# Performance work log

Measured on AMD Instinct MI355X. Metric: run time of the kernel, lower is better.

## Reference

```python
import jax, jax.numpy as jnp
import numpy as np

B, S, I, H = 8, 2048, 8, 256
HEADS, HD = 4, 64
DECAY = 0.95


def _lstm_layer(x, w_ih, w_hh, b_ih, b_hh):
    # x: [B, S, in]; torch gate order i, f, g, o
    Hs = w_hh.shape[1]
    x_proj = jnp.einsum('bsi,gi->bsg', x, w_ih) + b_ih + b_hh  # [B,S,4H]
    def step(carry, xt):
        h, c = carry
        gates = xt + h @ w_hh.T
        i, f, g, o = jnp.split(gates, 4, axis=-1)
        c = jax.nn.sigmoid(f) * c + jax.nn.sigmoid(i) * jnp.tanh(g)
        h = jax.nn.sigmoid(o) * jnp.tanh(c)
        return (h, c), h
    h0 = jnp.zeros((x.shape[0], Hs), x.dtype)
    (_, _), hs = jax.lax.scan(step, (h0, h0), jnp.swapaxes(x_proj, 0, 1))
    return jnp.swapaxes(hs, 0, 1)  # [B,S,H]


def setup_inputs() -> dict:
    key = jax.random.key(0)
    ks = jax.random.split(key, 25)
    sc = lambda n: 1.0 / np.sqrt(n)
    d = {}
    d['x'] = jax.random.normal(ks[0], (B, S, I), jnp.float32)
    # LSTM layer 0 (in=I) and layer 1 (in=H)
    d['w_ih0'] = jax.random.uniform(ks[1], (4 * H, I), jnp.float32, -sc(H), sc(H))
    d['w_hh0'] = jax.random.uniform(ks[2], (4 * H, H), jnp.float32, -sc(H), sc(H))
    d['b_ih0'] = jax.random.uniform(ks[3], (4 * H,), jnp.float32, -sc(H), sc(H))
    d['b_hh0'] = jax.random.uniform(ks[4], (4 * H,), jnp.float32, -sc(H), sc(H))
    d['w_ih1'] = jax.random.uniform(ks[5], (4 * H, H), jnp.float32, -sc(H), sc(H))
    d['w_hh1'] = jax.random.uniform(ks[6], (4 * H, H), jnp.float32, -sc(H), sc(H))
    d['b_ih1'] = jax.random.uniform(ks[7], (4 * H,), jnp.float32, -sc(H), sc(H))
    d['b_hh1'] = jax.random.uniform(ks[8], (4 * H,), jnp.float32, -sc(H), sc(H))
    # attention projections [H,H] (+bias)
    for i, n in enumerate(['q', 'k', 'v', 'o']):
        d['w' + n] = jax.random.normal(ks[9 + 2 * i], (H, H), jnp.float32) * sc(H)
        d['b' + n] = jnp.zeros((H,), jnp.float32)
    # dual heads [5,H]
    d['w_mean'] = jax.random.normal(ks[20], (5, H), jnp.float32) * sc(H)
    d['b_mean'] = jnp.zeros((5,), jnp.float32)
    d['w_var'] = jax.random.normal(ks[21], (5, H), jnp.float32) * sc(H)
    d['b_var'] = jnp.zeros((5,), jnp.float32)
    return d


def reference(x, w_ih0, w_hh0, b_ih0, b_hh0, w_ih1, w_hh1, b_ih1, b_hh1,
              wq, bq, wk, bk, wv, bv, wo, bo, w_mean, b_mean, w_var, b_var):
    # 2-layer LSTM (dropout between layers is identity in eval)
    h = _lstm_layer(x, w_ih0, w_hh0, b_ih0, b_hh0)
    h = _lstm_layer(h, w_ih1, w_hh1, b_ih1, b_hh1)  # [B,S,H]
    # temporal decay attention
    idx = jnp.arange(S)
    decay = DECAY ** jnp.abs(idx[None, :] - idx[:, None]).astype(jnp.float32)  # [S,S]
    def proj(w, b):
        return (h @ w.T + b).reshape(B, S, HEADS, HD).transpose(0, 2, 1, 3)
    q, k, v = proj(wq, bq), proj(wk, bk), proj(wv, bv)  # [B,He,S,HD]
    scores = jnp.einsum('bhqd,bhkd->bhqk', q, k) / np.sqrt(HD)
    scores = scores * decay  # multiplicative decay mask
    probs = jax.nn.softmax(scores, axis=-1)
    attn = jnp.einsum('bhqk,bhkd->bhqd', probs, v)
    attn = attn.transpose(0, 2, 1, 3).reshape(B, S, H)
    attn = attn @ wo.T + bo
    context = attn[:, -1, :]  # last token; dropout identity in eval
    mean = context @ w_mean.T + b_mean
    log_var = context @ w_var.T + b_var
    return (mean, log_var)
```

## Files before the change

kernel.cpp:

```cpp
#include <hip/hip_runtime.h>
#include <math.h>

#define BATCH 8
#define SEQ   2048
#define IN    8
#define HID   256
#define G4    1024
#define XPR_R 64

typedef unsigned long long u64;
typedef unsigned int u32;

__device__ __forceinline__ float sigmoidf_(float x) { return 1.0f / (1.0f + __expf(-x)); }
__device__ __forceinline__ float tanhf_(float x) { return 1.0f - 2.0f / (__expf(2.0f * x) + 1.0f); }
__device__ __forceinline__ int hpad(int k) { return k + 4 * (k >> 5); }

__device__ __forceinline__ void light_barrier() {
    __asm__ volatile("s_waitcnt lgkmcnt(0)\n\ts_barrier" ::: "memory");
}

__device__ __forceinline__ float dpp_add8(float v) {
    int x;
    x = __builtin_amdgcn_update_dpp(0, __float_as_int(v), 0xB1, 0xF, 0xF, false);
    v += __int_as_float(x);
    x = __builtin_amdgcn_update_dpp(0, __float_as_int(v), 0x4E, 0xF, 0xF, false);
    v += __int_as_float(x);
    x = __builtin_amdgcn_update_dpp(0, __float_as_int(v), 0x141, 0xF, 0xF, false);
    v += __int_as_float(x);
    return v;
}

__device__ __forceinline__ float poll_tag(const u64* p, u32 tag) {
    u64 v;
    do { v = __hip_atomic_load(p, __ATOMIC_RELAXED, __HIP_MEMORY_SCOPE_AGENT); }
    while ((u32)(v >> 32) != tag);
    return __uint_as_float((u32)v);
}
__device__ __forceinline__ void pub_tag(u64* p, u32 tag, float x) {
    __hip_atomic_store(p, ((u64)tag << 32) | (u64)__float_as_uint(x),
                       __ATOMIC_RELAXED, __HIP_MEMORY_SCOPE_AGENT);
}

__device__ __forceinline__ void matvec8(const float4 (&w4)[4][8], const float* hrow, int ks,
                                        float& a0, float& a1, float& a2, float& a3) {
    a0 = a1 = a2 = a3 = 0.0f;
#pragma unroll
    for (int i = 0; i < 8; i++) {
        const float4 h4 = *(const float4*)(&hrow[36 * ks + 4 * i]);
        a0 += w4[0][i].x*h4.x + w4[0][i].y*h4.y + w4[0][i].z*h4.z + w4[0][i].w*h4.w;
        a1 += w4[1][i].x*h4.x + w4[1][i].y*h4.y + w4[1][i].z*h4.z + w4[1][i].w*h4.w;
        a2 += w4[2][i].x*h4.x + w4[2][i].y*h4.y + w4[2][i].z*h4.z + w4[2][i].w*h4.w;
        a3 += w4[3][i].x*h4.x + w4[3][i].y*h4.y + w4[3][i].z*h4.z + w4[3][i].w*h4.w;
    }
}

__global__ __launch_bounds__(512, 2) void lstm_fused(
    const float* __restrict__ x,
    const float* __restrict__ w_ih0, const float* __restrict__ w_hh0,
    const float* __restrict__ b_ih0, const float* __restrict__ b_hh0,
    const float* __restrict__ w_ih1, const float* __restrict__ w_hh1,
    const float* __restrict__ b_ih1, const float* __restrict__ b_hh1,
    u64* __restrict__ h0s,
    u64* __restrict__ xpr,
    u64* __restrict__ h1r,
    float* __restrict__ hbuf)
{
    const int bid = blockIdx.x;
    const int b    = bid & 7;
    const int role = bid >> 3;
    const int grp  = role >> 2;
    const int q    = role & 3;
    const int t    = threadIdx.x;
    const int ks   = t & 7;
    const int rg   = t >> 3;
    const int wv   = t >> 6;
    const int lane = t & 63;
    const bool isg = (ks == 0);

    __shared__ float h_lds[2][288];
    __shared__ float xbuf[2][256];

    u64* h0b = h0s + (size_t)b * SEQ * HID;
    u64* xpb = xpr + (size_t)b * XPR_R * G4;

    for (int i = t; i < 576; i += 512) ((float*)h_lds)[i] = 0.0f;
    __syncthreads();

    if (grp == 0) {
        float4 w4[4][8];
#pragma unroll
        for (int j = 0; j < 4; j++) {
            const float4* wr = (const float4*)(w_hh0 + (size_t)(256*j + 64*q + rg) * HID + ks * 32);
#pragma unroll
            for (int i = 0; i < 8; i++) w4[j][i] = wr[i];
        }
        float4 wi[4][2]; float bs4[4];
#pragma unroll
        for (int j = 0; j < 4; j++) {
            const int G = 256*j + 64*q + rg;
            wi[j][0] = *(const float4*)(w_ih0 + (size_t)G * IN);
            wi[j][1] = *(const float4*)(w_ih0 + (size_t)G * IN + 4);
            bs4[j] = b_ih0[G] + b_hh0[G];
        }
        const float* xb = x + (size_t)b * SEQ * IN;
        float c = 0.0f;
        float xv0 = 0, xv1 = 0, xv2 = 0, xv3 = 0;
        if (isg) {
            const float4 xa = *(const float4*)(xb);
            const float4 xc = *(const float4*)(xb + 4);
            xv0 = bs4[0] + wi[0][0].x*xa.x + wi[0][0].y*xa.y + wi[0][0].z*xa.z + wi[0][0].w*xa.w
                         + wi[0][1].x*xc.x + wi[0][1].y*xc.y + wi[0][1].z*xc.z + wi[0][1].w*xc.w;
            xv1 = bs4[1] + wi[1][0].x*xa.x + wi[1][0].y*xa.y + wi[1][0].z*xa.z + wi[1][0].w*xa.w
                         + wi[1][1].x*xc.x + wi[1][1].y*xc.y + wi[1][1].z*xc.z + wi[1][1].w*xc.w;
            xv2 = bs4[2] + wi[2][0].x*xa.x + wi[2][0].y*xa.y + wi[2][0].z*xa.z + wi[2][0].w*xa.w
                         + wi[2][1].x*xc.x + wi[2][1].y*xc.y + wi[2][1].z*xc.z + wi[2][1].w*xc.w;
            xv3 = bs4[3] + wi[3][0].x*xa.x + wi[3][0].y*xa.y + wi[3][0].z*xa.z + wi[3][0].w*xa.w
                         + wi[3][1].x*xc.x + wi[3][1].y*xc.y + wi[3][1].z*xc.z + wi[3][1].w*xc.w;
        }

        for (int s = 0; s < SEQ; s++) {
            const int cur = s & 1, nxt = cur ^ 1;
            float xn0 = 0, xn1 = 0, xn2 = 0, xn3 = 0;
            if (isg && s + 1 < SEQ) {
                const float4 xa = *(const float4*)(xb + (size_t)(s + 1) * IN);
                const float4 xc = *(const float4*)(xb + (size_t)(s + 1) * IN + 4);
                xn0 = bs4[0] + wi[0][0].x*xa.x + wi[0][0].y*xa.y + wi[0][0].z*xa.z + wi[0][0].w*xa.w
                             + wi[0][1].x*xc.x + wi[0][1].y*xc.y + wi[0][1].z*xc.z + wi[0][1].w*xc.w;
                xn1 = bs4[1] + wi[1][0].x*xa.x + wi[1][0].y*xa.y + wi[1][0].z*xa.z + wi[1][0].w*xa.w
                             + wi[1][1].x*xc.x + wi[1][1].y*xc.y + wi[1][1].z*xc.z + wi[1][1].w*xc.w;
                xn2 = bs4[2] + wi[2][0].x*xa.x + wi[2][0].y*xa.y + wi[2][0].z*xa.z + wi[2][0].w*xa.w
                             + wi[2][1].x*xc.x + wi[2][1].y*xc.y + wi[2][1].z*xc.z + wi[2][1].w*xc.w;
                xn3 = bs4[3] + wi[3][0].x*xa.x + wi[3][0].y*xa.y + wi[3][0].z*xa.z + wi[3][0].w*xa.w
                             + wi[3][1].x*xc.x + wi[3][1].y*xc.y + wi[3][1].z*xc.z + wi[3][1].w*xc.w;
            }
            float a0, a1, a2, a3;
            matvec8(w4, h_lds[cur], ks, a0, a1, a2, a3);
            a0 = dpp_add8(a0); a1 = dpp_add8(a1); a2 = dpp_add8(a2); a3 = dpp_add8(a3);
            const u32 tag = (u32)(s + 1);
            if (isg) {
                const float iv = sigmoidf_(a0 + xv0);
                const float fv = sigmoidf_(a1 + xv1);
                const float gv = tanhf_(a2 + xv2);
                const float ov = sigmoidf_(a3 + xv3);
                c = fv * c + iv * gv;
                const float hv = ov * tanhf_(c);
                const int u = 64*q + rg;
                h_lds[nxt][hpad(u)] = hv;
                pub_tag(&h0b[(size_t)s * HID + u], tag, hv);
                xv0 = xn0; xv1 = xn1; xv2 = xn2; xv3 = xn3;
            }
            if (wv >= 1 && wv <= 3) {
                const int u = 64 * ((q + wv) & 3) + lane;
                h_lds[nxt][hpad(u)] = poll_tag(&h0b[(size_t)s * HID + u], tag);
            }
            light_barrier();
        }
    } else if (grp == 1) {
        const int p = q;
        float4 w4[4][8]; float bs4[4];
#pragma unroll
        for (int j = 0; j < 4; j++) {
            const int R = 256*p + 64*j + rg;
            const float4* wr = (const float4*)(w_ih1 + (size_t)R * HID + ks * 32);
#pragma unroll
            for (int i = 0; i < 8; i++) w4[j][i] = wr[i];
            bs4[j] = b_ih1[R] + b_hh1[R];
        }
        if (wv >= 4) {
            const int u = 64 * (wv - 4) + lane;
            h_lds[0][hpad(u)] = poll_tag(&h0b[u], 1u);
        }
        __syncthreads();

        for (int s = 0; s < SEQ; s++) {
            const int cur = s & 1, nxt = cur ^ 1;
            float a0, a1, a2, a3;
            matvec8(w4, h_lds[cur], ks, a0, a1, a2, a3);
            a0 = dpp_add8(a0); a1 = dpp_add8(a1); a2 = dpp_add8(a2); a3 = dpp_add8(a3);
            const u32 tag = (u32)(s + 1);
            if (isg) {
                if (s >= XPR_R) {
                    const u32 need = (u32)(s - (XPR_R - 1));
                    const u64* bp = h1r + ((size_t)(need & 1u) * 8 + b) * HID + (64*p + rg);
                    u32 tt;
                    do { tt = (u32)(__hip_atomic_load(bp, __ATOMIC_RELAXED, __HIP_MEMORY_SCOPE_AGENT) >> 32); }
                    while (!(tt >= need && tt <= 2048u));
                }
                u64* slot = xpb + (size_t)(s & (XPR_R - 1)) * G4 + 256*p + rg;
                pub_tag(slot +   0, tag, a0 + bs4[0]);
                pub_tag(slot +  64, tag, a1 + bs4[1]);
                pub_tag(slot + 128, tag, a2 + bs4[2]);
                pub_tag(slot + 192, tag, a3 + bs4[3]);
            }
            if (wv >= 4 && s + 1 < SEQ) {
                const int u = 64 * (wv - 4) + lane;
                h_lds[nxt][hpad(u)] = poll_tag(&h0b[(size_t)(s + 1) * HID + u], tag + 1u);
            }
            light_barrier();
        }
    } else {
        float4 w4[4][8];
#pragma unroll
        for (int j = 0; j < 4; j++) {
            const float4* wr = (const float4*)(w_hh1 + (size_t)(256*j + 64*q + rg) * HID + ks * 32);
#pragma unroll
            for (int i = 0; i < 8; i++) w4[j][i] = wr[i];
        }
        float* ho = hbuf + (size_t)b * SEQ * HID;
        if (wv >= 4) {
            const int j = wv - 4;
            xbuf[0][64*j + lane] = poll_tag(&xpb[256*j + 64*q + lane], 1u);
        }
        __syncthreads();

        float c = 0.0f;
        for (int s = 0; s < SEQ; s++) {
            const int cur = s & 1, nxt = cur ^ 1;
            float a0, a1, a2, a3;
            matvec8(w4, h_lds[cur], ks, a0, a1, a2, a3);
            a0 = dpp_add8(a0); a1 = dpp_add8(a1); a2 = dpp_add8(a2); a3 = dpp_add8(a3);
            const u32 tag = (u32)(s + 1);
            if (isg) {
                const float xq0 = xbuf[cur][rg];
                const float xq1 = xbuf[cur][64 + rg];
                const float xq2 = xbuf[cur][128 + rg];
                const float xq3 = xbuf[cur][192 + rg];
                const float iv = sigmoidf_(a0 + xq0);
                const float fv = sigmoidf_(a1 + xq1);
                const float gv = tanhf_(a2 + xq2);
                const float ov = sigmoidf_(a3 + xq3);
                c = fv * c + iv * gv;
                const float hv = ov * tanhf_(c);
                const int u = 64*q + rg;
                h_lds[nxt][hpad(u)] = hv;
                ho[(size_t)s * HID + u] = hv;
                pub_tag(&h1r[((size_t)(tag & 1u) * 8 + b) * HID + u], tag, hv);
            }
            if (wv >= 1 && wv <= 3) {
                const int u = 64 * ((q + wv) & 3) + lane;
                h_lds[nxt][hpad(u)] = poll_tag(&h1r[((size_t)(tag & 1u) * 8 + b) * HID + u], tag);
            }
            if (wv >= 4 && s + 1 < SEQ) {
                const int j = wv - 4;
                xbuf[nxt][64*j + lane] =
                    poll_tag(&xpb[(size_t)((s + 1) & (XPR_R - 1)) * G4 + 256*j + 64*q + lane], tag + 1u);
            }
            light_barrier();
        }
    }
}

__global__ __launch_bounds__(256) void gemm_kv(
    const float* __restrict__ A,
    const float* __restrict__ Wk, const float* __restrict__ bk,
    const float* __restrict__ Wv, const float* __restrict__ bv,
    float* __restrict__ Ck, float* __restrict__ Cv, int M, int N, int K)
{
    const float* W    = blockIdx.z ? Wv : Wk;
    const float* bias = blockIdx.z ? bv : bk;
    float*       C    = blockIdx.z ? Cv : Ck;

    __shared__ float As[16][132];
    __shared__ float Bs[16][132];
    const int tid = threadIdx.x;
    const int tx = tid & 15;
    const int ty = tid >> 4;
    const int bm = blockIdx.x * 128;
    const int bn = blockIdx.y * 128;
    const int lrow = tid >> 1;
    const int lk = (tid & 1) * 8;

    float acc[8][8] = {};

    for (int k0 = 0; k0 < K; k0 += 16) {
        const float* ap = A + (size_t)(bm + lrow) * K + k0 + lk;
        const float* wp = W + (size_t)(bn + lrow) * K + k0 + lk;
        const float4 a0 = *(const float4*)ap;
        const float4 a1 = *(const float4*)(ap + 4);
        const float4 w0 = *(const float4*)wp;
        const float4 w1 = *(const float4*)(wp + 4);
        __syncthreads();
        As[lk+0][lrow] = a0.x; As[lk+1][lrow] = a0.y; As[lk+2][lrow] = a0.z; As[lk+3][lrow] = a0.w;
        As[lk+4][lrow] = a1.x; As[lk+5][lrow] = a1.y; As[lk+6][lrow] = a1.z; As[lk+7][lrow] = a1.w;
        Bs[lk+0][lrow] = w0.x; Bs[lk+1][lrow] = w0.y; Bs[lk+2][lrow] = w0.z; Bs[lk+3][lrow] = w0.w;
        Bs[lk+4][lrow] = w1.x; Bs[lk+5][lrow] = w1.y; Bs[lk+6][lrow] = w1.z; Bs[lk+7][lrow] = w1.w;
        __syncthreads();
#pragma unroll
        for (int k = 0; k < 16; k++) {
            const float4 av0 = *(const float4*)(&As[k][ty * 4]);
            const float4 av1 = *(const float4*)(&As[k][64 + ty * 4]);
            const float4 bv0 = *(const float4*)(&Bs[k][tx * 4]);
            const float4 bv1 = *(const float4*)(&Bs[k][64 + tx * 4]);
            const float ar[8] = {av0.x, av0.y, av0.z, av0.w, av1.x, av1.y, av1.z, av1.w};
            const float br[8] = {bv0.x, bv0.y, bv0.z, bv0.w, bv1.x, bv1.y, bv1.z, bv1.w};
#pragma unroll
            for (int i = 0; i < 8; i++)
#pragma unroll
                for (int j = 0; j < 8; j++) acc[i][j] += ar[i] * br[j];
        }
    }

    const int c0 = bn + tx * 4, c1 = bn + 64 + tx * 4;
    const float4 bb0 = *(const float4*)(bias + c0);
    const float4 bb1 = *(const float4*)(bias + c1);
#pragma unroll
    for (int ih = 0; ih < 2; ih++)
#pragma unroll
        for (int i = 0; i < 4; i++) {
            const int row = bm + ih * 64 + ty * 4 + i;
            const int ai = ih * 4 + i;
            float4 o0, o1;
            o0.x = acc[ai][0] + bb0.x; o0.y = acc[ai][1] + bb0.y;
            o0.z = acc[ai][2] + bb0.z; o0.w = acc[ai][3] + bb0.w;
            o1.x = acc[ai][4] + bb1.x; o1.y = acc[ai][5] + bb1.y;
            o1.z = acc[ai][6] + bb1.z; o1.w = acc[ai][7] + bb1.w;
            *(float4*)(C + (size_t)row * N + c0) = o0;
            *(float4*)(C + (size_t)row * N + c1) = o1;
        }
}

__global__ __launch_bounds__(256) void qlast_kernel(
    const float* __restrict__ h1, const float* __restrict__ wq,
    const float* __restrict__ bq, float* __restrict__ qout)
{
    const int b = blockIdx.x;
    const int t = threadIdx.x;
    __shared__ __align__(16) float hs[HID];
    hs[t] = h1[((size_t)b * SEQ + (SEQ - 1)) * HID + t];
    __syncthreads();
    const float4* wr = (const float4*)(wq + (size_t)t * HID);
    float acc = 0.0f;
#pragma unroll
    for (int k = 0; k < 64; k++) {
        const float4 wv = wr[k];
        const float4 hv = ((const float4*)hs)[k];
        acc += wv.x*hv.x + wv.y*hv.y + wv.z*hv.z + wv.w*hv.w;
    }
    qout[b * HID + t] = acc + bq[t];
}

__global__ __launch_bounds__(256) void attn_kernel(
    const float* __restrict__ Kb, const float* __restrict__ Vb,
    const float* __restrict__ q, float* __restrict__ attn)
{
    const int b = blockIdx.x >> 2;
    const int h = blockIdx.x & 3;
    const int tid = threadIdx.x;

    __shared__ __align__(16) float qs[64];
    __shared__ float sc[SEQ];
    __shared__ float red[256];
    __shared__ float part[4][64];

    if (tid < 64) qs[tid] = q[b * HID + h * 64 + tid];
    __syncthreads();

    const float LN095 = -0.051293294387550533f;
    for (int k = tid; k < SEQ; k += 256) {
        const float4* kr = (const float4*)(Kb + ((size_t)b * SEQ + k) * HID + h * 64);
        float acc = 0.0f;
#pragma unroll
        for (int d = 0; d < 16; d++) {
            const float4 kv = kr[d];
            const float4 qv = ((const float4*)qs)[d];
            acc += kv.x*qv.x + kv.y*qv.y + kv.z*qv.z + kv.w*qv.w;
        }
        const float dec = __expf(LN095 * (float)(SEQ - 1 - k));
        sc[k] = acc * 0.125f * dec;
    }
    __syncthreads();

    float m = -INFINITY;
    for (int k = tid; k < SEQ; k += 256) m = fmaxf(m, sc[k]);
    red[tid] = m;
    for (int off = 128; off > 0; off >>= 1) {
        __syncthreads();
        if (tid < off) red[tid] = fmaxf(red[tid], red[tid + off]);
    }
    __syncthreads();
    const float mx = red[0];

    float local = 0.0f;
    for (int k = tid; k < SEQ; k += 256) {
        const float p = expf(sc[k] - mx);
        sc[k] = p;
        local += p;
    }
    __syncthreads();
    red[tid] = local;
    for (int off = 128; off > 0; off >>= 1) {
        __syncthreads();
        if (tid < off) red[tid] += red[tid + off];
    }
    __syncthreads();
    const float total = red[0];

    const int chunk = tid >> 6;
    const int d = tid & 63;
    float acc = 0.0f;
    const int k0 = chunk * (SEQ / 4), k1 = (chunk + 1) * (SEQ / 4);
    for (int k = k0; k < k1; k++)
        acc += sc[k] * Vb[((size_t)b * SEQ + k) * HID + h * 64 + d];
    part[chunk][d] = acc;
    __syncthreads();
    if (tid < 64) {
        const float r = (part[0][tid] + part[1][tid]) + (part[2][tid] + part[3][tid]);
        attn[b * HID + h * 64 + tid] = r / total;
    }
}

__global__ __launch_bounds__(256) void head_kernel(
    const float* __restrict__ attn, const float* __restrict__ wo,
    const float* __restrict__ bo, const float* __restrict__ w_mean,
    const float* __restrict__ b_mean, const float* __restrict__ w_var,
    const float* __restrict__ b_var, float* __restrict__ out)
{
    const int b = blockIdx.x;
    const int t = threadIdx.x;
    __shared__ __align__(16) float av[HID];
    __shared__ __align__(16) float ctx[HID];
    av[t] = attn[b * HID + t];
    __syncthreads();
    {
        const float4* wr = (const float4*)(wo + (size_t)t * HID);
        float acc = 0.0f;
#pragma unroll
        for (int k = 0; k < 64; k++) {
            const float4 wv = wr[k];
            const float4 hv = ((const float4*)av)[k];
            acc += wv.x*hv.x + wv.y*hv.y + wv.z*hv.z + wv.w*hv.w;
        }
        ctx[t] = acc + bo[t];
    }
    __syncthreads();
    if (t < 5) {
        const float4* wr = (const float4*)(w_mean + (size_t)t * HID);
        float acc = 0.0f;
#pragma unroll
        for (int k = 0; k < 64; k++) {
            const float4 wv = wr[k];
            const float4 hv = ((const float4*)ctx)[k];
            acc += wv.x*hv.x + wv.y*hv.y + wv.z*hv.z + wv.w*hv.w;
        }
        out[b * 5 + t] = acc + b_mean[t];
    } else if (t >= 8 && t < 13) {
        const int m = t - 8;
        const float4* wr = (const float4*)(w_var + (size_t)m * HID);
        float acc = 0.0f;
#pragma unroll
        for (int k = 0; k < 64; k++) {
            const float4 wv = wr[k];
            const float4 hv = ((const float4*)ctx)[k];
            acc += wv.x*hv.x + wv.y*hv.y + wv.z*hv.z + wv.w*hv.w;
        }
        out[BATCH * 5 + b * 5 + m] = acc + b_var[m];
    }
}

extern "C" void kernel_launch(void* const* d_in, const int* in_sizes, int n_in,
                              void* d_out, int out_size, void* d_ws, size_t ws_size,
                              hipStream_t stream) {
    const float* x      = (const float*)d_in[0];
    const float* w_ih0  = (const float*)d_in[1];
    const float* w_hh0  = (const float*)d_in[2];
    const float* b_ih0  = (const float*)d_in[3];
    const float* b_hh0  = (const float*)d_in[4];
    const float* w_ih1  = (const float*)d_in[5];
    const float* w_hh1  = (const float*)d_in[6];
    const float* b_ih1  = (const float*)d_in[7];
    const float* b_hh1  = (const float*)d_in[8];
    const float* wq     = (const float*)d_in[9];
    const float* bq     = (const float*)d_in[10];
    const float* wk     = (const float*)d_in[11];
    const float* bk     = (const float*)d_in[12];
    const float* wvv    = (const float*)d_in[13];
    const float* bv     = (const float*)d_in[14];
    const float* wo     = (const float*)d_in[15];
    const float* bo     = (const float*)d_in[16];
    const float* w_mean = (const float*)d_in[17];
    const float* b_mean = (const float*)d_in[18];
    const float* w_var  = (const float*)d_in[19];
    const float* b_var  = (const float*)d_in[20];
    float* out = (float*)d_out;

    char* wsb = (char*)d_ws;
    u64*  h0s  = (u64*)(wsb);
    u64*  xpr  = (u64*)(wsb + 33554432);
    u64*  h1r  = (u64*)(wsb + 37748736);
    float* hbuf = (float*)(wsb + 37781504);
    float* Kbuf = (float*)(wsb);
    float* Vbuf = (float*)(wsb + 16777216);
    float* qbuf = (float*)(wsb + 33554432);
    float* abuf = (float*)(wsb + 33554432 + 8192);

    lstm_fused<<<96, 512, 0, stream>>>(x, w_ih0, w_hh0, b_ih0, b_hh0,
                                       w_ih1, w_hh1, b_ih1, b_hh1,
                                       h0s, xpr, h1r, hbuf);
    gemm_kv<<<dim3(128, 2, 2), 256, 0, stream>>>(hbuf, wk, bk, wvv, bv, Kbuf, Vbuf, 16384, 256, 256);
    qlast_kernel<<<BATCH, 256, 0, stream>>>(hbuf, wq, bq, qbuf);
    attn_kernel<<<BATCH * 4, 256, 0, stream>>>(Kbuf, Vbuf, qbuf, abuf);
    head_kernel<<<BATCH, 256, 0, stream>>>(abuf, wo, bo, w_mean, b_mean, w_var, b_var, out);
}
```

Before: 3.603 ms.

## Restructure LSTM blocks to 256 threads with per-wave K-split and LDS partial sums

Blocks shrink from 512 to 256 threads, and the matvec is reorganised. Each wave now owns a 64-wide slice of the hidden-state input with weights held in registers as float2 vectors. Partial sums are reduced through shared memory instead of DPP across 8 lanes. A dedicated wave does the gate math and publishes h while the other waves poll remote slices. This aims to cut per-step latency on the serial recurrence and to use packed FMA, at the cost of higher register pressure and an extra LDS reduction step.

New measurement: 4.587 ms. +27.3%, slower.

```diff
diff --git a/kernel.cpp b/kernel.cpp
--- a/kernel.cpp
+++ b/kernel.cpp
@@ -10,24 +10,13 @@
 
 typedef unsigned long long u64;
 typedef unsigned int u32;
+typedef float v2f __attribute__((ext_vector_type(2)));
 
 __device__ __forceinline__ float sigmoidf_(float x) { return 1.0f / (1.0f + __expf(-x)); }
 __device__ __forceinline__ float tanhf_(float x) { return 1.0f - 2.0f / (__expf(2.0f * x) + 1.0f); }
-__device__ __forceinline__ int hpad(int k) { return k + 4 * (k >> 5); }
 
 __device__ __forceinline__ void light_barrier() {
     __asm__ volatile("s_waitcnt lgkmcnt(0)\n\ts_barrier" ::: "memory");
-}
-
-__device__ __forceinline__ float dpp_add8(float v) {
-    int x;
-    x = __builtin_amdgcn_update_dpp(0, __float_as_int(v), 0xB1, 0xF, 0xF, false);
-    v += __int_as_float(x);
-    x = __builtin_amdgcn_update_dpp(0, __float_as_int(v), 0x4E, 0xF, 0xF, false);
-    v += __int_as_float(x);
-    x = __builtin_amdgcn_update_dpp(0, __float_as_int(v), 0x141, 0xF, 0xF, false);
-    v += __int_as_float(x);
-    return v;
 }
 
 __device__ __forceinline__ float poll_tag(const u64* p, u32 tag) {
@@ -41,20 +30,7 @@
                        __ATOMIC_RELAXED, __HIP_MEMORY_SCOPE_AGENT);
 }
 
-__device__ __forceinline__ void matvec8(const float4 (&w4)[4][8], const float* hrow, int ks,
-                                        float& a0, float& a1, float& a2, float& a3) {
-    a0 = a1 = a2 = a3 = 0.0f;
-#pragma unroll
-    for (int i = 0; i < 8; i++) {
-        const float4 h4 = *(const float4*)(&hrow[36 * ks + 4 * i]);
-        a0 += w4[0][i].x*h4.x + w4[0][i].y*h4.y + w4[0][i].z*h4.z + w4[0][i].w*h4.w;
-        a1 += w4[1][i].x*h4.x + w4[1][i].y*h4.y + w4[1][i].z*h4.z + w4[1][i].w*h4.w;
-        a2 += w4[2][i].x*h4.x + w4[2][i].y*h4.y + w4[2][i].z*h4.z + w4[2][i].w*h4.w;
-        a3 += w4[3][i].x*h4.x + w4[3][i].y*h4.y + w4[3][i].z*h4.z + w4[3][i].w*h4.w;
-    }
-}
-
-__global__ __launch_bounds__(512, 2) void lstm_fused(
+__global__ __launch_bounds__(256, 1) void lstm_fused(
     const float* __restrict__ x,
     const float* __restrict__ w_ih0, const float* __restrict__ w_hh0,
     const float* __restrict__ b_ih0, const float* __restrict__ b_hh0,
@@ -65,187 +41,176 @@
     u64* __restrict__ h1r,
     float* __restrict__ hbuf)
 {
-    const int bid = blockIdx.x;
+    const int bid  = blockIdx.x;
     const int b    = bid & 7;
     const int role = bid >> 3;
     const int grp  = role >> 2;
     const int q    = role & 3;
     const int t    = threadIdx.x;
-    const int ks   = t & 7;
-    const int rg   = t >> 3;
     const int wv   = t >> 6;
     const int lane = t & 63;
-    const bool isg = (ks == 0);
-
-    __shared__ float h_lds[2][288];
-    __shared__ float xbuf[2][256];
+
+    __shared__ float cb[4][64];
+    __shared__ float part[2][4][4][64];
 
     u64* h0b = h0s + (size_t)b * SEQ * HID;
     u64* xpb = xpr + (size_t)b * XPR_R * G4;
 
-    for (int i = t; i < 576; i += 512) ((float*)h_lds)[i] = 0.0f;
-    __syncthreads();
-
-    if (grp == 0) {
-        float4 w4[4][8];
+    ((float*)cb)[t] = 0.0f;
+    __syncthreads();
+
+    if (grp == 1) {
+        const int p = q;
+        v2f w2[4][32];
 #pragma unroll
         for (int j = 0; j < 4; j++) {
-            const float4* wr = (const float4*)(w_hh0 + (size_t)(256*j + 64*q + rg) * HID + ks * 32);
-#pragma unroll
-            for (int i = 0; i < 8; i++) w4[j][i] = wr[i];
-        }
-        float4 wi[4][2]; float bs4[4];
+            const v2f* wr = (const v2f*)(w_ih1 + (size_t)(256*p + 64*j + lane) * HID + 64*wv);
+#pragma unroll
+            for (int i = 0; i < 32; i++) w2[j][i] = wr[i];
+        }
+        const int myrow  = 256*p + 64*wv + lane;
+        const int myunit = 64*wv + lane;
+        const float bs = b_ih1[myrow] + b_hh1[myrow];
+
+        for (int s = 0; s < SEQ; s++) {
+            const int par = s & 1;
+            cb[wv][lane] = poll_tag(&h0b[(size_t)s * HID + 64*wv + lane], (u32)(s + 1));
+            v2f a0 = {0,0}, a1 = {0,0}, a2 = {0,0}, a3 = {0,0};
+#pragma unroll
+            for (int i = 0; i < 16; i++) {
+                const float4 h4 = *(const float4*)&cb[wv][4*i];
+                const v2f h01 = {h4.x, h4.y}, h23 = {h4.z, h4.w};
+                a0 = w2[0][2*i]*h01 + a0; a0 = w2[0][2*i+1]*h23 + a0;
+                a1 = w2[1][2*i]*h01 + a1; a1 = w2[1][2*i+1]*h23 + a1;
+                a2 = w2[2][2*i]*h01 + a2; a2 = w2[2][2*i+1]*h23 + a2;
+                a3 = w2[3][2*i]*h01 + a3; a3 = w2[3][2*i+1]*h23 + a3;
+            }
+            part[par][wv][0][lane] = a0.x + a0.y;
+            part[par][wv][1][lane] = a1.x + a1.y;
+            part[par][wv][2][lane] = a2.x + a2.y;
+            part[par][wv][3][lane] = a3.x + a3.y;
+            light_barrier();
+            const float g = part[par][0][wv][lane] + part[par][1][wv][lane]
+                          + part[par][2][wv][lane] + part[par][3][wv][lane] + bs;
+            if (s >= XPR_R) {
+                const u32 need = (u32)(s - (XPR_R - 1));
+                const u64* bp = &h1r[((size_t)(need & 1u) * 8 + b) * HID + myunit];
+                u32 tt;
+                do { tt = (u32)(__hip_atomic_load(bp, __ATOMIC_RELAXED, __HIP_MEMORY_SCOPE_AGENT) >> 32); }
+                while (!(tt >= need && tt <= 2048u));
+            }
+            pub_tag(&xpb[(size_t)(s & (XPR_R - 1)) * G4 + myrow], (u32)(s + 1), g);
+        }
+    } else {
+        const int cw = (wv == 3) ? q : ((q + 1 + wv) & 3);
+        const float* whh = (grp == 0) ? w_hh0 : w_hh1;
+        v2f w2[4][32];
 #pragma unroll
         for (int j = 0; j < 4; j++) {
-            const int G = 256*j + 64*q + rg;
-            wi[j][0] = *(const float4*)(w_ih0 + (size_t)G * IN);
-            wi[j][1] = *(const float4*)(w_ih0 + (size_t)G * IN + 4);
-            bs4[j] = b_ih0[G] + b_hh0[G];
-        }
+            const v2f* wr = (const v2f*)(whh + (size_t)(256*j + 64*q + lane) * HID + 64*cw);
+#pragma unroll
+            for (int i = 0; i < 32; i++) w2[j][i] = wr[i];
+        }
+
+        float4 wia[4], wib[4]; float bs4[4];
+        float xv0 = 0, xv1 = 0, xv2 = 0, xv3 = 0;
         const float* xb = x + (size_t)b * SEQ * IN;
+        float* ho = hbuf + (size_t)b * SEQ * HID;
+        if (wv == 3) {
+            if (grp == 0) {
+#pragma unroll
+                for (int j = 0; j < 4; j++) {
+                    const int G = 256*j + 64*q + lane;
+                    wia[j] = *(const float4*)(w_ih0 + (size_t)G * IN);
+                    wib[j] = *(const float4*)(w_ih0 + (size_t)G * IN + 4);
+                    bs4[j] = b_ih0[G] + b_hh0[G];
+                }
+                const float4 xa = *(const float4*)(xb);
+                const float4 xc = *(const float4*)(xb + 4);
+                xv0 = bs4[0] + wia[0].x*xa.x + wia[0].y*xa.y + wia[0].z*xa.z + wia[0].w*xa.w
+                             + wib[0].x*xc.x + wib[0].y*xc.y + wib[0].z*xc.z + wib[0].w*xc.w;
+                xv1 = bs4[1] + wia[1].x*xa.x + wia[1].y*xa.y + wia[1].z*xa.z + wia[1].w*xa.w
+                             + wib[1].x*xc.x + wib[1].y*xc.y + wib[1].z*xc.z + wib[1].w*xc.w;
+                xv2 = bs4[2] + wia[2].x*xa.x + wia[2].y*xa.y + wia[2].z*xa.z + wia[2].w*xa.w
+                             + wib[2].x*xc.x + wib[2].y*xc.y + wib[2].z*xc.z + wib[2].w*xc.w;
+                xv3 = bs4[3] + wia[3].x*xa.x + wia[3].y*xa.y + wia[3].z*xa.z + wia[3].w*xa.w
+                             + wib[3].x*xc.x + wib[3].y*xc.y + wib[3].z*xc.z + wib[3].w*xc.w;
+            } else {
+                const int u = 64*q + lane;
+                xv0 = poll_tag(&xpb[0*G4 + 0   + u], 1u);
+                xv1 = poll_tag(&xpb[0*G4 + 256 + u], 1u);
+                xv2 = poll_tag(&xpb[0*G4 + 512 + u], 1u);
+                xv3 = poll_tag(&xpb[0*G4 + 768 + u], 1u);
+            }
+        }
+
         float c = 0.0f;
-        float xv0 = 0, xv1 = 0, xv2 = 0, xv3 = 0;
-        if (isg) {
-            const float4 xa = *(const float4*)(xb);
-            const float4 xc = *(const float4*)(xb + 4);
-            xv0 = bs4[0] + wi[0][0].x*xa.x + wi[0][0].y*xa.y + wi[0][0].z*xa.z + wi[0][0].w*xa.w
-                         + wi[0][1].x*xc.x + wi[0][1].y*xc.y + wi[0][1].z*xc.z + wi[0][1].w*xc.w;
-            xv1 = bs4[1] + wi[1][0].x*xa.x + wi[1][0].y*xa.y + wi[1][0].z*xa.z + wi[1][0].w*xa.w
-                         + wi[1][1].x*xc.x + wi[1][1].y*xc.y + wi[1][1].z*xc.z + wi[1][1].w*xc.w;
-            xv2 = bs4[2] + wi[2][0].x*xa.x + wi[2][0].y*xa.y + wi[2][0].z*xa.z + wi[2][0].w*xa.w
-                         + wi[2][1].x*xc.x + wi[2][1].y*xc.y + wi[2][1].z*xc.z + wi[2][1].w*xc.w;
-            xv3 = bs4[3] + wi[3][0].x*xa.x + wi[3][0].y*xa.y + wi[3][0].z*xa.z + wi[3][0].w*xa.w
-                         + wi[3][1].x*xc.x + wi[3][1].y*xc.y + wi[3][1].z*xc.z + wi[3][1].w*xc.w;
-        }
-
         for (int s = 0; s < SEQ; s++) {
-            const int cur = s & 1, nxt = cur ^ 1;
-            float xn0 = 0, xn1 = 0, xn2 = 0, xn3 = 0;
-            if (isg && s + 1 < SEQ) {
-                const float4 xa = *(const float4*)(xb + (size_t)(s + 1) * IN);
-                const float4 xc = *(const float4*)(xb + (size_t)(s + 1) * IN + 4);
-                xn0 = bs4[0] + wi[0][0].x*xa.x + wi[0][0].y*xa.y + wi[0][0].z*xa.z + wi[0][0].w*xa.w
-                             + wi[0][1].x*xc.x + wi[0][1].y*xc.y + wi[0][1].z*xc.z + wi[0][1].w*xc.w;
-                xn1 = bs4[1] + wi[1][0].x*xa.x + wi[1][0].y*xa.y + wi[1][0].z*xa.z + wi[1][0].w*xa.w
-                             + wi[1][1].x*xc.x + wi[1][1].y*xc.y + wi[1][1].z*xc.z + wi[1][1].w*xc.w;
-                xn2 = bs4[2] + wi[2][0].x*xa.x + wi[2][0].y*xa.y + wi[2][0].z*xa.z + wi[2][0].w*xa.w
-                             + wi[2][1].x*xc.x + wi[2][1].y*xc.y + wi[2][1].z*xc.z + wi[2][1].w*xc.w;
-                xn3 = bs4[3] + wi[3][0].x*xa.x + wi[3][0].y*xa.y + wi[3][0].z*xa.z + wi[3][0].w*xa.w
-                             + wi[3][1].x*xc.x + wi[3][1].y*xc.y + wi[3][1].z*xc.z + wi[3][1].w*xc.w;
-            }
-            float a0, a1, a2, a3;
-            matvec8(w4, h_lds[cur], ks, a0, a1, a2, a3);
-            a0 = dpp_add8(a0); a1 = dpp_add8(a1); a2 = dpp_add8(a2); a3 = dpp_add8(a3);
-            const u32 tag = (u32)(s + 1);
-            if (isg) {
-                const float iv = sigmoidf_(a0 + xv0);
-                const float fv = sigmoidf_(a1 + xv1);
-                const float gv = tanhf_(a2 + xv2);
-                const float ov = sigmoidf_(a3 + xv3);
+            const int par = s & 1;
+            if (wv < 3 && s > 0) {
+                const u64* src = (grp == 0)
+                    ? &h0b[(size_t)(s - 1) * HID + 64*cw + lane]
+                    : &h1r[((size_t)(s & 1u) * 8 + b) * HID + 64*cw + lane];
+                cb[cw][lane] = poll_tag(src, (u32)s);
+            }
+            v2f a0 = {0,0}, a1 = {0,0}, a2 = {0,0}, a3 = {0,0};
+#pragma unroll
+            for (int i = 0; i < 16; i++) {
+                const float4 h4 = *(const float4*)&cb[cw][4*i];
+                const v2f h01 = {h4.x, h4.y}, h23 = {h4.z, h4.w};
+                a0 = w2[0][2*i]*h01 + a0; a0 = w2[0][2*i+1]*h23 + a0;
+                a1 = w2[1][2*i]*h01 + a1; a1 = w2[1][2*i+1]*h23 + a1;
+                a2 = w2[2][2*i]*h01 + a2; a2 = w2[2][2*i+1]*h23 + a2;
+                a3 = w2[3][2*i]*h01 + a3; a3 = w2[3][2*i+1]*h23 + a3;
+            }
+            part[par][cw][0][lane] = a0.x + a0.y;
+            part[par][cw][1][lane] = a1.x + a1.y;
+            part[par][cw][2][lane] = a2.x + a2.y;
+            part[par][cw][3][lane] = a3.x + a3.y;
+            light_barrier();
+            if (wv == 3) {
+                const float g0 = part[par][0][0][lane] + part[par][1][0][lane]
+                               + part[par][2][0][lane] + part[par][3][0][lane];
+                const float g1 = part[par][0][1][lane] + part[par][1][1][lane]
+                               + part[par][2][1][lane] + part[par][3][1][lane];
+                const float g2 = part[par][0][2][lane] + part[par][1][2][lane]
+                               + part[par][2][2][lane] + part[par][3][2][lane];
+                const float g3 = part[par][0][3][lane] + part[par][1][3][lane]
+                               + part[par][2][3][lane] + part[par][3][3][lane];
+                const float iv = sigmoidf_(g0 + xv0);
+                const float fv = sigmoidf_(g1 + xv1);
+                const float gv = tanhf_(g2 + xv2);
+                const float ov = sigmoidf_(g3 + xv3);
                 c = fv * c + iv * gv;
                 const float hv = ov * tanhf_(c);
-                const int u = 64*q + rg;
-                h_lds[nxt][hpad(u)] = hv;
-                pub_tag(&h0b[(size_t)s * HID + u], tag, hv);
-                xv0 = xn0; xv1 = xn1; xv2 = xn2; xv3 = xn3;
-            }
-            if (wv >= 1 && wv <= 3) {
-                const int u = 64 * ((q + wv) & 3) + lane;
-                h_lds[nxt][hpad(u)] = poll_tag(&h0b[(size_t)s * HID + u], tag);
-            }
-            light_barrier();
-        }
-    } else if (grp == 1) {
-        const int p = q;
-        float4 w4[4][8]; float bs4[4];
-#pragma unroll
-        for (int j = 0; j < 4; j++) {
-            const int R = 256*p + 64*j + rg;
-            const float4* wr = (const float4*)(w_ih1 + (size_t)R * HID + ks * 32);
-#pragma unroll
-            for (int i = 0; i < 8; i++) w4[j][i] = wr[i];
-            bs4[j] = b_ih1[R] + b_hh1[R];
-        }
-        if (wv >= 4) {
-            const int u = 64 * (wv - 4) + lane;
-            h_lds[0][hpad(u)] = poll_tag(&h0b[u], 1u);
-        }
-        __syncthreads();
-
-        for (int s = 0; s < SEQ; s++) {
-            const int cur = s & 1, nxt = cur ^ 1;
-            float a0, a1, a2, a3;
-            matvec8(w4, h_lds[cur], ks, a0, a1, a2, a3);
-            a0 = dpp_add8(a0); a1 = dpp_add8(a1); a2 = dpp_add8(a2); a3 = dpp_add8(a3);
-            const u32 tag = (u32)(s + 1);
-            if (isg) {
-                if (s >= XPR_R) {
-                    const u32 need = (u32)(s - (XPR_R - 1));
-                    const u64* bp = h1r + ((size_t)(need & 1u) * 8 + b) * HID + (64*p + rg);
-                    u32 tt;
-                    do { tt = (u32)(__hip_atomic_load(bp, __ATOMIC_RELAXED, __HIP_MEMORY_SCOPE_AGENT) >> 32); }
-                    while (!(tt >= need && tt <= 2048u));
+                const int u = 64*q + lane;
+                cb[q][lane] = hv;
+                if (grp == 0) {
+                    pub_tag(&h0b[(size_t)s * HID + u], (u32)(s + 1), hv);
+                    if (s + 1 < SEQ) {
+                        const float4 xa = *(const float4*)(xb + (size_t)(s + 1) * IN);
+                        const float4 xc = *(const float4*)(xb + (size_t)(s + 1) * IN + 4);
+                        xv0 = bs4[0] + wia[0].x*xa.x + wia[0].y*xa.y + wia[0].z*xa.z + wia[0].w*xa.w
+                                     + wib[0].x*xc.x + wib[0].y*xc.y + wib[0].z*xc.z + wib[0].w*xc.w;
+                        xv1 = bs4[1] + wia[1].x*xa.x + wia[1].y*xa.y + wia[1].z*xa.z + wia[1].w*xa.w
+                                     + wib[1].x*xc.x + wib[1].y*xc.y + wib[1].z*xc.z + wib[1].w*xc.w;
+                        xv2 = bs4[2] + wia[2].x*xa.x + wia[2].y*xa.y + wia[2].z*xa.z + wia[2].w*xa.w
+                                     + wib[2].x*xc.x + wib[2].y*xc.y + wib[2].z*xc.z + wib[2].w*xc.w;
+                        xv3 = bs4[3] + wia[3].x*xa.x + wia[3].y*xa.y + wia[3].z*xa.z + wia[3].w*xa.w
+                                     + wib[3].x*xc.x + wib[3].y*xc.y + wib[3].z*xc.z + wib[3].w*xc.w;
+                    }
+                } else {
+                    ho[(size_t)s * HID + u] = hv;
+                    pub_tag(&h1r[((size_t)((s + 1) & 1u) * 8 + b) * HID + u], (u32)(s + 1), hv);
+                    if (s + 1 < SEQ) {
+                        const size_t sl = (size_t)((s + 1) & (XPR_R - 1)) * G4;
+                        xv0 = poll_tag(&xpb[sl + 0   + u], (u32)(s + 2));
+                        xv1 = poll_tag(&xpb[sl + 256 + u], (u32)(s + 2));
+                        xv2 = poll_tag(&xpb[sl + 512 + u], (u32)(s + 2));
+                        xv3 = poll_tag(&xpb[sl + 768 + u], (u32)(s + 2));
+                    }
                 }
-                u64* slot = xpb + (size_t)(s & (XPR_R - 1)) * G4 + 256*p + rg;
-                pub_tag(slot +   0, tag, a0 + bs4[0]);
-                pub_tag(slot +  64, tag, a1 + bs4[1]);
-                pub_tag(slot + 128, tag, a2 + bs4[2]);
-                pub_tag(slot + 192, tag, a3 + bs4[3]);
-            }
-            if (wv >= 4 && s + 1 < SEQ) {
-                const int u = 64 * (wv - 4) + lane;
-                h_lds[nxt][hpad(u)] = poll_tag(&h0b[(size_t)(s + 1) * HID + u], tag + 1u);
-            }
-            light_barrier();
-        }
-    } else {
-        float4 w4[4][8];
-#pragma unroll
-        for (int j = 0; j < 4; j++) {
-            const float4* wr = (const float4*)(w_hh1 + (size_t)(256*j + 64*q + rg) * HID + ks * 32);
-#pragma unroll
-            for (int i = 0; i < 8; i++) w4[j][i] = wr[i];
-        }
-        float* ho = hbuf + (size_t)b * SEQ * HID;
-        if (wv >= 4) {
-            const int j = wv - 4;
-            xbuf[0][64*j + lane] = poll_tag(&xpb[256*j + 64*q + lane], 1u);
-        }
-        __syncthreads();
-
-        float c = 0.0f;
-        for (int s = 0; s < SEQ; s++) {
-            const int cur = s & 1, nxt = cur ^ 1;
-            float a0, a1, a2, a3;
-            matvec8(w4, h_lds[cur], ks, a0, a1, a2, a3);
-            a0 = dpp_add8(a0); a1 = dpp_add8(a1); a2 = dpp_add8(a2); a3 = dpp_add8(a3);
-            const u32 tag = (u32)(s + 1);
-            if (isg) {
-                const float xq0 = xbuf[cur][rg];
-                const float xq1 = xbuf[cur][64 + rg];
-                const float xq2 = xbuf[cur][128 + rg];
-                const float xq3 = xbuf[cur][192 + rg];
-                const float iv = sigmoidf_(a0 + xq0);
-                const float fv = sigmoidf_(a1 + xq1);
-                const float gv = tanhf_(a2 + xq2);
-                const float ov = sigmoidf_(a3 + xq3);
-                c = fv * c + iv * gv;
-                const float hv = ov * tanhf_(c);
-                const int u = 64*q + rg;
-                h_lds[nxt][hpad(u)] = hv;
-                ho[(size_t)s * HID + u] = hv;
-                pub_tag(&h1r[((size_t)(tag & 1u) * 8 + b) * HID + u], tag, hv);
-            }
-            if (wv >= 1 && wv <= 3) {
-                const int u = 64 * ((q + wv) & 3) + lane;
-                h_lds[nxt][hpad(u)] = poll_tag(&h1r[((size_t)(tag & 1u) * 8 + b) * HID + u], tag);
-            }
-            if (wv >= 4 && s + 1 < SEQ) {
-                const int j = wv - 4;
-                xbuf[nxt][64*j + lane] =
-                    poll_tag(&xpb[(size_t)((s + 1) & (XPR_R - 1)) * G4 + 256*j + 64*q + lane], tag + 1u);
-            }
-            light_barrier();
+            }
         }
     }
 }
@@ -493,7 +458,7 @@
     float* qbuf = (float*)(wsb + 33554432);
     float* abuf = (float*)(wsb + 33554432 + 8192);
 
-    lstm_fused<<<96, 512, 0, stream>>>(x, w_ih0, w_hh0, b_ih0, b_hh0,
+    lstm_fused<<<96, 256, 0, stream>>>(x, w_ih0, w_hh0, b_ih0, b_hh0,
                                        w_ih1, w_hh1, b_ih1, b_hh1,
                                        h0s, xpr, h1r, hbuf);
     gemm_kv<<<dim3(128, 2, 2), 256, 0, stream>>>(hbuf, wk, bk, wvv, bv, Kbuf, Vbuf, 16384, 256, 256);
```
